# Kernel optimization log

Measured on AMD Instinct MI355X. Metric: run time of the kernel, lower is better.

The kernel has to match this reference:

```python
import jax, jax.numpy as jnp
import numpy as np
from jax import lax

# SRCNN: conv 9x9 (1->64) + ReLU, conv 5x5 (64->32) + ReLU, conv 5x5 (32->1), same padding.
# 13 units total: indices 0-3 (x2 stage), 4-7 (x4 stage), 8-11 (x8 stage), 12 (msf).

def _conv(x, w, b):
    y = lax.conv_general_dilated(x, w, window_strides=(1, 1), padding='SAME',
                                 dimension_numbers=('NCHW', 'OIHW', 'NCHW'))
    return y + b[None, :, None, None]


def _srcnn(x, w1, b1, w2, b2, w3, b3):
    h = jax.nn.relu(_conv(x, w1, b1))
    h = jax.nn.relu(_conv(h, w2, b2))
    return _conv(h, w3, b3)


def _interleave(p0, p1, p2, p3):
    # out[b,c,2h,2w]=p0, out[b,c,2h,2w+1]=p1, out[b,c,2h+1,2w]=p2, out[b,c,2h+1,2w+1]=p3
    B, C, H, W = p0.shape
    x = jnp.stack([jnp.stack([p0, p1], axis=-1),
                   jnp.stack([p2, p3], axis=-1)], axis=-2)  # (B,C,H,W,2,2) dims (b,c,h,w,r,s)
    x = x.transpose(0, 1, 2, 4, 3, 5)                        # (b,c,h,r,w,s)
    return x.reshape(B, C, 2 * H, 2 * W)


def _stage(x, off, W1, B1, W2, B2, W3, B3):
    outs = [_srcnn(x, W1[off + i], B1[off + i], W2[off + i], B2[off + i],
                   W3[off + i], B3[off + i]) for i in range(4)]
    return _interleave(*outs)


def _upscale(x, s):
    B, C, H, W = x.shape
    return jax.image.resize(x, (B, C, H * s, W * s), method='bilinear')


def setup_inputs() -> dict:
    key = jax.random.key(0)
    ks = jax.random.split(key, 7)
    image = jax.random.normal(ks[0], (4, 1, 64, 64), dtype=jnp.float32)
    n = 13
    W1 = jax.random.normal(ks[1], (n, 64, 1, 9, 9), dtype=jnp.float32) * 0.05
    B1 = jnp.zeros((n, 64), dtype=jnp.float32)
    W2 = jax.random.normal(ks[2], (n, 32, 64, 5, 5), dtype=jnp.float32) * 0.05
    B2 = jnp.zeros((n, 32), dtype=jnp.float32)
    W3 = jax.random.normal(ks[3], (n, 1, 32, 5, 5), dtype=jnp.float32) * 0.05
    B3 = jnp.zeros((n, 1), dtype=jnp.float32)
    return {'image': image, 'W1': W1, 'B1': B1, 'W2': W2, 'B2': B2, 'W3': W3, 'B3': B3}


def reference(image, W1, B1, W2, B2, W3, B3):
    out_x2 = _stage(image, 0, W1, B1, W2, B2, W3, B3)   # (B,1,128,128)
    out_x4 = _stage(out_x2, 4, W1, B1, W2, B2, W3, B3)  # (B,1,256,256)
    out_x8 = _stage(out_x4, 8, W1, B1, W2, B2, W3, B3)  # (B,1,512,512)
    msf_in = _upscale(out_x2, 4) + _upscale(out_x4, 2) + out_x8
    msf_out = _srcnn(msf_in, W1[12], B1[12], W2[12], B2[12], W3[12], B3[12])
    return (out_x2, out_x4, out_x8, msf_out)
```

## Files before the change

### kernel.cpp

```cpp
#include <hip/hip_runtime.h>


typedef unsigned short ushort_t;
typedef __attribute__((ext_vector_type(8))) short short8;
typedef __attribute__((ext_vector_type(4))) float f32x4;
typedef __attribute__((ext_vector_type(2))) unsigned int u32x2;

__device__ __forceinline__ float us2f(ushort_t u) { return __uint_as_float(((unsigned int)u) << 16); }
__device__ __forceinline__ ushort_t f2us(float f) {
    unsigned int x = __float_as_uint(f);
    return (ushort_t)((x + 0x7fffu + ((x >> 16) & 1u)) >> 16);
}
__device__ __forceinline__ unsigned int pk_bf16(float lo, float hi) {
    unsigned int r;
    asm("v_cvt_pk_bf16_f32 %0, %1, %2" : "=v"(r) : "v"(lo), "v"(hi));
    return r;
}

#define MFMA16(a, b, c) __builtin_amdgcn_mfma_f32_16x16x32_bf16((a), (b), (c), 0, 0, 0)

__global__ __launch_bounds__(256) void prep_weights(
    const float* __restrict__ W1, const float* __restrict__ W2, const float* __restrict__ W3,
    ushort_t* __restrict__ w1t, ushort_t* __restrict__ w2t, ushort_t* __restrict__ w3t)
{
    int i = blockIdx.x * 256 + threadIdx.x;
    if (i < 13 * 3 * 4 * 64 * 8) {
        int e = i & 7, ch = (i >> 3) & 63, cig = (i >> 9) & 3;
        int r = i >> 11;
        int kc = r % 3, u = r / 3;
        int tap = kc * 32 + e * 4 + cig;
        w1t[i] = (tap < 81) ? f2us(W1[(u * 64 + ch) * 81 + tap]) : (ushort_t)0;
    }
    if (i < 532480) {
        int e = i & 7, co = (i >> 3) & 31, qq = (i >> 8) & 3;
        int b = i >> 10;
        int dy = b % 5, tt = b / 5;
        int c8 = tt % 8, u = tt / 8;
        int ci = c8 * 8 + e;
        int tap = dy * 5 + qq;
        w2t[i] = f2us(W2[((u * 32 + co) * 64 + ci) * 25 + tap]);
    }
    if (i < 133120) {
        int e = i & 7, co = (i >> 3) & 31, cig = (i >> 8) & 3;
        int b = i >> 10;
        int dy = b % 5, s = b / 5;
        int c = s % 2, u = s / 2;
        int ci = c * 32 + cig * 8 + e;
        int tap = dy * 5 + 4;
        w2t[532480 + i] = f2us(W2[((u * 32 + co) * 64 + ci) * 25 + tap]);
    }
    if (i < 13 * 25 * 32) {
        int ci = i & 31, r = i >> 5;
        int tap = r % 25, u = r / 25;
        w3t[i] = f2us(W3[(u * 32 + ci) * 25 + tap]);
    }
}

__global__ __launch_bounds__(256, 2) void srcnn_mfma(
    const float* __restrict__ in, int H, int W,
    const ushort_t* __restrict__ w1t, const ushort_t* __restrict__ w2t,
    const ushort_t* __restrict__ w3t,
    const float* __restrict__ gB1, const float* __restrict__ gB2,
    const float* __restrict__ gB3,
    int unitBase, float* __restrict__ out, int s2)
{
    __shared__ __align__(16) char smem[52928];
    ushort_t* sH1  = (ushort_t*)smem;
    ushort_t* sInU = (ushort_t*)(smem + 51328);
    ushort_t* sW3  = (ushort_t*)(smem + 51328);
    ushort_t* sH2  = (ushort_t*)smem;

    const int t = threadIdx.x, lane = t & 63, wv = t >> 6;
    const int q = lane >> 4, l15 = lane & 15;
    const int z = blockIdx.z;
    const int k4 = (s2 == 2) ? (z >> 2) : 0;
    const int b  = (s2 == 2) ? (z & 3)  : z;
    const int unit = unitBase + k4;
    const int ppx = k4 & 1, ppy = k4 >> 1;
    const int ox0 = blockIdx.x * 12, oy0 = blockIdx.y * 12;
    const int outW = W * s2;
    const int outH = H * s2;
    const float* inb = in + (size_t)b * H * W;

    const char* w2m_u = (const char*)w2t + (size_t)unit * 81920;
    const char* w2x_u = (const char*)w2t + 1064960 + (size_t)unit * 20480;

    auto loadW = [&](short8* buf, const char* base, int blk) {
        const char* g = base + (size_t)blk * 10240 + q * 512 + l15 * 16;
#pragma unroll
        for (int dy = 0; dy < 5; ++dy) {
            buf[dy]     = *(const short8*)(g + dy * 2048);
            buf[5 + dy] = *(const short8*)(g + dy * 2048 + 256);
        }
    };

    for (int idx = t; idx < 784; idx += 256) {
        int y = idx / 28, x = idx - 28 * y;
        int gy = oy0 - 8 + y, gx = ox0 - 8 + x;
        sInU[idx] = (gy >= 0 && gy < H && gx >= 0 && gx < W)
                    ? f2us(inb[(size_t)gy * W + gx]) : (ushort_t)0;
    }
    __syncthreads();

    const ushort_t* w1u = w1t + (size_t)unit * (3 * 4 * 64 * 8);

    f32x4 bias4[4];
#pragma unroll
    for (int n = 0; n < 4; ++n)
        bias4[n] = *(const f32x4*)&gB1[unit * 64 + n * 16 + q * 4];

#pragma unroll 1
    for (int ms = 0; ms < 2; ++ms) {
        const int mbase = ms * 16;
        const int nim = ms ? 3 : 4;
        f32x4 acc1h[4][4];
#pragma unroll
        for (int i = 0; i < 4; ++i)
#pragma unroll
            for (int n = 0; n < 4; ++n) acc1h[i][n] = (f32x4){0.f, 0.f, 0.f, 0.f};

#pragma unroll 1
        for (int kc = 0; kc < 3; ++kc) {
            short8 bh[4];
#pragma unroll
            for (int n = 0; n < 4; ++n)
                bh[n] = *(const short8*)&w1u[((kc * 4 + q) * 64 + n * 16 + l15) * 8];
            int toff8[8];
#pragma unroll
            for (int j = 0; j < 8; ++j) {
                int T = kc * 32 + j * 4 + q;
                int ty = (T * 57) >> 9;
                int o  = ty * 28 + (T - 9 * ty);
                toff8[j] = (T < 81) ? o : 0;
            }
#pragma unroll
            for (int im = 0; im < 4; ++im) {
                if (im < nim) {
                    int m = mbase + wv + im * 4;
                    if (m < 25) {
                        int px = m * 16 + l15;
                        int py1 = (px * 205) >> 12;
                        int base = py1 * 28 + (px - 20 * py1);
                        union { short8 v; ushort_t u[8]; } a;
#pragma unroll
                        for (int j = 0; j < 8; ++j)
                            a.u[j] = sInU[base + toff8[j]];
#pragma unroll
                        for (int n = 0; n < 4; ++n)
                            acc1h[im][n] = MFMA16(bh[n], a.v, acc1h[im][n]);
                    }
                }
            }
        }

#pragma unroll
        for (int im = 0; im < 4; ++im) {
            if (im < nim) {
                int m = mbase + wv + im * 4;
                if (m < 25) {
                    int px = m * 16 + l15;
                    int py1 = (px * 205) >> 12;
                    int px1 = px - 20 * py1;
                    int gy = oy0 - 4 + py1, gx = ox0 - 4 + px1;
                    bool ok = (gy >= 0 && gy < H && gx >= 0 && gx < W);
#pragma unroll
                    for (int n = 0; n < 4; ++n) {
                        float v0 = fmaxf(acc1h[im][n][0] + bias4[n][0], 0.f);
                        float v1 = fmaxf(acc1h[im][n][1] + bias4[n][1], 0.f);
                        float v2 = fmaxf(acc1h[im][n][2] + bias4[n][2], 0.f);
                        float v3 = fmaxf(acc1h[im][n][3] + bias4[n][3], 0.f);
                        unsigned int w0 = pk_bf16(v0, v1);
                        unsigned int w1 = pk_bf16(v2, v3);
                        if (!ok) { w0 = 0u; w1 = 0u; }
                        *(u32x2*)&sH1[(n * 2 + (q >> 1)) * 3208 + px * 8 + (q & 1) * 4]
                            = (u32x2){w0, w1};
                    }
                }
            }
        }
    }
    __syncthreads();

    {
        const ushort_t* w3u = w3t + unit * 800;
        for (int i = t; i < 800; i += 256) sW3[i] = w3u[i];
    }

    f32x4 acc2[4][2];
#pragma unroll
    for (int i = 0; i < 4; ++i) { acc2[i][0] = (f32x4){0.f,0.f,0.f,0.f}; acc2[i][1] = (f32x4){0.f,0.f,0.f,0.f}; }

    {
        short8 Wa[10], Wb[10];
        loadW(Wa, w2m_u, 0);
#pragma unroll
        for (int c8 = 0; c8 < 8; ++c8) {
            const short8* cw = (c8 & 1) ? Wb : Wa;
            short8*       nw = (c8 & 1) ? Wa : Wb;
            if (c8 < 7) loadW(nw, w2m_u, c8 + 1);
            else        loadW(nw, w2x_u, 0);
            const ushort_t* bpl = &sH1[c8 * 3208];
#pragma unroll
            for (int rel = 0; rel < 8; ++rel) {
                int row = wv * 4 + rel;
                short8 bf = *(const short8*)&bpl[(row * 20 + l15 + q) * 8];
                const int dylo = rel - 3 < 0 ? 0 : rel - 3;
                const int dyhi = rel < 4 ? rel : 4;
#pragma unroll
                for (int dy = 0; dy < 5; ++dy) {
                    if (dy >= dylo && dy <= dyhi) {
                        int im = rel - dy;
                        acc2[im][0] = MFMA16(cw[dy],     bf, acc2[im][0]);
                        acc2[im][1] = MFMA16(cw[5 + dy], bf, acc2[im][1]);
                    }
                }
            }
        }
#pragma unroll
        for (int c = 0; c < 2; ++c) {
            const short8* cw = (c & 1) ? Wb : Wa;
            short8*       nw = (c & 1) ? Wa : Wb;
            if (c == 0) loadW(nw, w2x_u, 1);
            const ushort_t* base = &sH1[(c * 4 + q) * 3208];
#pragma unroll
            for (int rel = 0; rel < 8; ++rel) {
                int row = wv * 4 + rel;
                short8 bf = *(const short8*)&base[(row * 20 + l15 + 4) * 8];
                const int dylo = rel - 3 < 0 ? 0 : rel - 3;
                const int dyhi = rel < 4 ? rel : 4;
#pragma unroll
                for (int dy = 0; dy < 5; ++dy) {
                    if (dy >= dylo && dy <= dyhi) {
                        int im = rel - dy;
                        acc2[im][0] = MFMA16(cw[dy],     bf, acc2[im][0]);
                        acc2[im][1] = MFMA16(cw[5 + dy], bf, acc2[im][1]);
                    }
                }
            }
        }
    }
    __syncthreads();

    {
        f32x4 b2v[2];
#pragma unroll
        for (int n = 0; n < 2; ++n)
            b2v[n] = *(const f32x4*)&gB2[unit * 32 + n * 16 + q * 4];
        int gx = ox0 - 2 + l15;
        bool okx = (gx >= 0 && gx < W);
#pragma unroll
        for (int im = 0; im < 4; ++im) {
            int hy = wv * 4 + im;
            int gy = oy0 - 2 + hy;
            bool ok = okx && (gy >= 0 && gy < H);
#pragma unroll
            for (int n = 0; n < 2; ++n) {
                float v0 = fmaxf(acc2[im][n][0] + b2v[n][0], 0.f);
                float v1 = fmaxf(acc2[im][n][1] + b2v[n][1], 0.f);
                float v2 = fmaxf(acc2[im][n][2] + b2v[n][2], 0.f);
                float v3 = fmaxf(acc2[im][n][3] + b2v[n][3], 0.f);
                unsigned int w0 = pk_bf16(v0, v1);
                unsigned int w1 = pk_bf16(v2, v3);
                if (!ok) { w0 = 0u; w1 = 0u; }
                *(u32x2*)&sH2[(n * 2 + (q >> 1)) * 2064 + (hy * 16 + l15) * 8 + (q & 1) * 4]
                    = (u32x2){w0, w1};
            }
        }
    }
    __syncthreads();

    float b3 = gB3[unit];
    const int nm = (wv == 0) ? 3 : 2;
    int oyj[3], oxj[3];
#pragma unroll
    for (int jm = 0; jm < 3; ++jm) {
        int p = (wv + 4 * jm) * 16 + l15;
        oyj[jm] = (p * 683) >> 13;
        oxj[jm] = p - 12 * oyj[jm];
    }
    f32x4 acc3[3];
#pragma unroll
    for (int jm = 0; jm < 3; ++jm) acc3[jm] = (f32x4){0.f, 0.f, 0.f, 0.f};

#pragma unroll 1
    for (int tap = 0; tap < 25; ++tap) {
        int dy = (tap * 13) >> 6, dx = tap - 5 * dy;
        short8 w = *(const short8*)&sW3[tap * 32 + q * 8];
#pragma unroll
        for (int jm = 0; jm < 3; ++jm) {
            if (jm < nm) {
                int h2px = (oyj[jm] + dy) * 16 + oxj[jm] + dx;
                short8 a = *(const short8*)&sH2[q * 2064 + h2px * 8];
                acc3[jm] = MFMA16(a, w, acc3[jm]);
            }
        }
    }
    if (l15 == 0) {
#pragma unroll
        for (int jm = 0; jm < 3; ++jm) {
            if (jm < nm) {
                int mt = wv + 4 * jm;
#pragma unroll
                for (int r = 0; r < 4; ++r) {
                    int pp = mt * 16 + q * 4 + r;
                    int oy = (pp * 683) >> 13, ox = pp - 12 * oy;
                    int gy = oy0 + oy, gx = ox0 + ox;
                    if (gy < H && gx < W) {
                        size_t o = (size_t)b * outW * outH + (size_t)(gy * s2 + ppy) * outW + (gx * s2 + ppx);
                        out[o] = acc3[jm][r] + b3;
                    }
                }
            }
        }
    }
}

__device__ __forceinline__ void ax_w(int i, float inv_s, int n, int& i0, int& i1, float& w1) {
    float c  = (i + 0.5f) * inv_s - 0.5f;
    float fl = floorf(c);
    w1 = c - fl;
    int ii = (int)fl;
    i0 = ii < 0 ? 0 : ii;
    i1 = (ii + 1 >= n) ? (n - 1) : (ii + 1);
}

__global__ __launch_bounds__(256) void msf_in_kernel(
    const float* __restrict__ f2, const float* __restrict__ f4,
    const float* __restrict__ f8, float* __restrict__ dst)
{
    int idx = blockIdx.x * 256 + threadIdx.x;
    int x = idx & 511;
    int y = (idx >> 9) & 511;
    int b = idx >> 18;

    int y0, y1, x0, x1;
    float wy, wx;

    ax_w(y, 0.25f, 128, y0, y1, wy);
    ax_w(x, 0.25f, 128, x0, x1, wx);
    const float* p2 = f2 + (size_t)b * 16384;
    float v4 = (1.f - wy) * ((1.f - wx) * p2[y0 * 128 + x0] + wx * p2[y0 * 128 + x1])
             +        wy  * ((1.f - wx) * p2[y1 * 128 + x0] + wx * p2[y1 * 128 + x1]);

    ax_w(y, 0.5f, 256, y0, y1, wy);
    ax_w(x, 0.5f, 256, x0, x1, wx);
    const float* p4 = f4 + (size_t)b * 65536;
    float v2 = (1.f - wy) * ((1.f - wx) * p4[y0 * 256 + x0] + wx * p4[y0 * 256 + x1])
             +        wy  * ((1.f - wx) * p4[y1 * 256 + x0] + wx * p4[y1 * 256 + x1]);

    dst[idx] = v4 + v2 + f8[idx];
}

extern "C" void kernel_launch(void* const* d_in, const int* in_sizes, int n_in,
                              void* d_out, int out_size, void* d_ws, size_t ws_size,
                              hipStream_t stream)
{
    (void)in_sizes; (void)n_in; (void)out_size; (void)ws_size;

    const float* image = (const float*)d_in[0];
    const float* W1    = (const float*)d_in[1];
    const float* B1    = (const float*)d_in[2];
    const float* W2    = (const float*)d_in[3];
    const float* B2    = (const float*)d_in[4];
    const float* W3    = (const float*)d_in[5];
    const float* B3    = (const float*)d_in[6];

    float* out = (float*)d_out;
    float* o2 = out;
    float* o4 = out + 65536;
    float* o8 = out + 327680;
    float* om = out + 1376256;

    float*    fm  = (float*)d_ws;
    ushort_t* w1t = (ushort_t*)((char*)d_ws + 4194304);
    ushort_t* w2t = (ushort_t*)((char*)d_ws + 4354048);
    ushort_t* w3t = (ushort_t*)((char*)d_ws + 5685248);

    prep_weights<<<2600, 256, 0, stream>>>(W1, W2, W3, w1t, w2t, w3t);

    srcnn_mfma<<<dim3(6, 6, 16), 256, 0, stream>>>(
        image, 64, 64, w1t, w2t, w3t, B1, B2, B3, 0, o2, 2);
    srcnn_mfma<<<dim3(11, 11, 16), 256, 0, stream>>>(
        o2, 128, 128, w1t, w2t, w3t, B1, B2, B3, 4, o4, 2);
    srcnn_mfma<<<dim3(22, 22, 16), 256, 0, stream>>>(
        o4, 256, 256, w1t, w2t, w3t, B1, B2, B3, 8, o8, 2);
    msf_in_kernel<<<4096, 256, 0, stream>>>(o2, o4, o8, fm);
    srcnn_mfma<<<dim3(43, 43, 4), 256, 0, stream>>>(
        fm, 512, 512, w1t, w2t, w3t, B1, B2, B3, 12, om, 1);
}
```

Before: 626.1 us.

## Double block to 512 threads and split conv2 output channels across wave halves

```diff
diff --git a/kernel.cpp b/kernel.cpp
--- a/kernel.cpp
+++ b/kernel.cpp
@@ -56,7 +56,7 @@
     }
 }
 
-__global__ __launch_bounds__(256, 2) void srcnn_mfma(
+__global__ __launch_bounds__(512, 2) void srcnn_mfma(
     const float* __restrict__ in, int H, int W,
     const ushort_t* __restrict__ w1t, const ushort_t* __restrict__ w2t,
     const ushort_t* __restrict__ w3t,
@@ -72,6 +72,7 @@
 
     const int t = threadIdx.x, lane = t & 63, wv = t >> 6;
     const int q = lane >> 4, l15 = lane & 15;
+    const int wp = wv & 3, nh = wv >> 2;
     const int z = blockIdx.z;
     const int k4 = (s2 == 2) ? (z >> 2) : 0;
     const int b  = (s2 == 2) ? (z & 3)  : z;
@@ -85,16 +86,14 @@
     const char* w2m_u = (const char*)w2t + (size_t)unit * 81920;
     const char* w2x_u = (const char*)w2t + 1064960 + (size_t)unit * 20480;
 
-    auto loadW = [&](short8* buf, const char* base, int blk) {
-        const char* g = base + (size_t)blk * 10240 + q * 512 + l15 * 16;
-#pragma unroll
-        for (int dy = 0; dy < 5; ++dy) {
-            buf[dy]     = *(const short8*)(g + dy * 2048);
-            buf[5 + dy] = *(const short8*)(g + dy * 2048 + 256);
-        }
+    auto loadW5 = [&](short8* buf, const char* base, int blk) {
+        const char* g = base + (size_t)blk * 10240 + q * 512 + nh * 256 + l15 * 16;
+#pragma unroll
+        for (int dy = 0; dy < 5; ++dy)
+            buf[dy] = *(const short8*)(g + dy * 2048);
     };
 
-    for (int idx = t; idx < 784; idx += 256) {
+    for (int idx = t; idx < 784; idx += 512) {
         int y = idx / 28, x = idx - 28 * y;
         int gy = oy0 - 8 + y, gx = ox0 - 8 + x;
         sInU[idx] = (gy >= 0 && gy < H && gx >= 0 && gx < W)
@@ -109,10 +108,8 @@
     for (int n = 0; n < 4; ++n)
         bias4[n] = *(const f32x4*)&gB1[unit * 64 + n * 16 + q * 4];
 
-#pragma unroll 1
-    for (int ms = 0; ms < 2; ++ms) {
-        const int mbase = ms * 16;
-        const int nim = ms ? 3 : 4;
+    const int nim1 = (wv == 0) ? 4 : 3;
+    {
         f32x4 acc1h[4][4];
 #pragma unroll
         for (int i = 0; i < 4; ++i)
@@ -135,46 +132,42 @@
             }
 #pragma unroll
             for (int im = 0; im < 4; ++im) {
-                if (im < nim) {
-                    int m = mbase + wv + im * 4;
-                    if (m < 25) {
-                        int px = m * 16 + l15;
-                        int py1 = (px * 205) >> 12;
-                        int base = py1 * 28 + (px - 20 * py1);
-                        union { short8 v; ushort_t u[8]; } a;
-#pragma unroll
-                        for (int j = 0; j < 8; ++j)
-                            a.u[j] = sInU[base + toff8[j]];
-#pragma unroll
-                        for (int n = 0; n < 4; ++n)
-                            acc1h[im][n] = MFMA16(bh[n], a.v, acc1h[im][n]);
-                    }
-                }
-            }
-        }
-
-#pragma unroll
-        for (int im = 0; im < 4; ++im) {
-            if (im < nim) {
-                int m = mbase + wv + im * 4;
-                if (m < 25) {
+                if (im < nim1) {
+                    int m = wv + im * 8;
                     int px = m * 16 + l15;
                     int py1 = (px * 205) >> 12;
-                    int px1 = px - 20 * py1;
-                    int gy = oy0 - 4 + py1, gx = ox0 - 4 + px1;
-                    bool ok = (gy >= 0 && gy < H && gx >= 0 && gx < W);
-#pragma unroll
-                    for (int n = 0; n < 4; ++n) {
-                        float v0 = fmaxf(acc1h[im][n][0] + bias4[n][0], 0.f);
-                        float v1 = fmaxf(acc1h[im][n][1] + bias4[n][1], 0.f);
-                        float v2 = fmaxf(acc1h[im][n][2] + bias4[n][2], 0.f);
-                        float v3 = fmaxf(acc1h[im][n][3] + bias4[n][3], 0.f);
-                        unsigned int w0 = pk_bf16(v0, v1);
-                        unsigned int w1 = pk_bf16(v2, v3);
-                        if (!ok) { w0 = 0u; w1 = 0u; }
-                        *(u32x2*)&sH1[(n * 2 + (q >> 1)) * 3208 + px * 8 + (q & 1) * 4]
-                            = (u32x2){w0, w1};
-                    }
+                    int base = py1 * 28 + (px - 20 * py1);
+                    union { short8 v; ushort_t u[8]; } a;
+#pragma unroll
+                    for (int j = 0; j < 8; ++j)
+                        a.u[j] = sInU[base + toff8[j]];
+#pragma unroll
+                    for (int n = 0; n < 4; ++n)
+                        acc1h[im][n] = MFMA16(bh[n], a.v, acc1h[im][n]);
+                }
+            }
+        }
+
+#pragma unroll
+        for (int im = 0; im < 4; ++im) {
+            if (im < nim1) {
+                int m = wv + im * 8;
+                int px = m * 16 + l15;
+                int py1 = (px * 205) >> 12;
+                int px1 = px - 20 * py1;
+                int gy = oy0 - 4 + py1, gx = ox0 - 4 + px1;
+                bool ok = (gy >= 0 && gy < H && gx >= 0 && gx < W);
+#pragma unroll
+                for (int n = 0; n < 4; ++n) {
+                    float v0 = fmaxf(acc1h[im][n][0] + bias4[n][0], 0.f);
+                    float v1 = fmaxf(acc1h[im][n][1] + bias4[n][1], 0.f);
+                    float v2 = fmaxf(acc1h[im][n][2] + bias4[n][2], 0.f);
+                    float v3 = fmaxf(acc1h[im][n][3] + bias4[n][3], 0.f);
+                    unsigned int w0 = pk_bf16(v0, v1);
+                    unsigned int w1 = pk_bf16(v2, v3);
+                    if (!ok) { w0 = 0u; w1 = 0u; }
+                    *(u32x2*)&sH1[(n * 2 + (q >> 1)) * 3208 + px * 8 + (q & 1) * 4]
+                        = (u32x2){w0, w1};
                 }
             }
         }
@@ -183,26 +176,26 @@
 
     {
         const ushort_t* w3u = w3t + unit * 800;
-        for (int i = t; i < 800; i += 256) sW3[i] = w3u[i];
-    }
-
-    f32x4 acc2[4][2];
-#pragma unroll
-    for (int i = 0; i < 4; ++i) { acc2[i][0] = (f32x4){0.f,0.f,0.f,0.f}; acc2[i][1] = (f32x4){0.f,0.f,0.f,0.f}; }
+        for (int i = t; i < 800; i += 512) sW3[i] = w3u[i];
+    }
+
+    f32x4 acc2[4];
+#pragma unroll
+    for (int i = 0; i < 4; ++i) acc2[i] = (f32x4){0.f, 0.f, 0.f, 0.f};
 
     {
-        short8 Wa[10], Wb[10];
-        loadW(Wa, w2m_u, 0);
+        short8 Wa[5], Wb[5];
+        loadW5(Wa, w2m_u, 0);
 #pragma unroll
         for (int c8 = 0; c8 < 8; ++c8) {
             const short8* cw = (c8 & 1) ? Wb : Wa;
             short8*       nw = (c8 & 1) ? Wa : Wb;
-            if (c8 < 7) loadW(nw, w2m_u, c8 + 1);
-            else        loadW(nw, w2x_u, 0);
+            if (c8 < 7) loadW5(nw, w2m_u, c8 + 1);
+            else        loadW5(nw, w2x_u, 0);
             const ushort_t* bpl = &sH1[c8 * 3208];
 #pragma unroll
             for (int rel = 0; rel < 8; ++rel) {
-                int row = wv * 4 + rel;
+                int row = wp * 4 + rel;
                 short8 bf = *(const short8*)&bpl[(row * 20 + l15 + q) * 8];
                 const int dylo = rel - 3 < 0 ? 0 : rel - 3;
                 const int dyhi = rel < 4 ? rel : 4;
@@ -210,8 +203,7 @@
                 for (int dy = 0; dy < 5; ++dy) {
                     if (dy >= dylo && dy <= dyhi) {
                         int im = rel - dy;
-                        acc2[im][0] = MFMA16(cw[dy],     bf, acc2[im][0]);
-                        acc2[im][1] = MFMA16(cw[5 + dy], bf, acc2[im][1]);
+                        acc2[im] = MFMA16(cw[dy], bf, acc2[im]);
                     }
                 }
             }
@@ -220,11 +212,11 @@
         for (int c = 0; c < 2; ++c) {
             const short8* cw = (c & 1) ? Wb : Wa;
             short8*       nw = (c & 1) ? Wa : Wb;
-            if (c == 0) loadW(nw, w2x_u, 1);
+            if (c == 0) loadW5(nw, w2x_u, 1);
             const ushort_t* base = &sH1[(c * 4 + q) * 3208];
 #pragma unroll
             for (int rel = 0; rel < 8; ++rel) {
-                int row = wv * 4 + rel;
+                int row = wp * 4 + rel;
                 short8 bf = *(const short8*)&base[(row * 20 + l15 + 4) * 8];
                 const int dylo = rel - 3 < 0 ? 0 : rel - 3;
                 const int dyhi = rel < 4 ? rel : 4;
@@ -232,8 +224,7 @@
                 for (int dy = 0; dy < 5; ++dy) {
                     if (dy >= dylo && dy <= dyhi) {
                         int im = rel - dy;
-                        acc2[im][0] = MFMA16(cw[dy],     bf, acc2[im][0]);
-                        acc2[im][1] = MFMA16(cw[5 + dy], bf, acc2[im][1]);
+                        acc2[im] = MFMA16(cw[dy], bf, acc2[im]);
                     }
                 }
             }
@@ -242,52 +233,46 @@
     __syncthreads();
 
     {
-        f32x4 b2v[2];
-#pragma unroll
-        for (int n = 0; n < 2; ++n)
-            b2v[n] = *(const f32x4*)&gB2[unit * 32 + n * 16 + q * 4];
+        f32x4 b2v = *(const f32x4*)&gB2[unit * 32 + nh * 16 + q * 4];
         int gx = ox0 - 2 + l15;
         bool okx = (gx >= 0 && gx < W);
 #pragma unroll
         for (int im = 0; im < 4; ++im) {
-            int hy = wv * 4 + im;
+            int hy = wp * 4 + im;
             int gy = oy0 - 2 + hy;
             bool ok = okx && (gy >= 0 && gy < H);
-#pragma unroll
-            for (int n = 0; n < 2; ++n) {
-                float v0 = fmaxf(acc2[im][n][0] + b2v[n][0], 0.f);
-                float v1 = fmaxf(acc2[im][n][1] + b2v[n][1], 0.f);
-                float v2 = fmaxf(acc2[im][n][2] + b2v[n][2], 0.f);
-                float v3 = fmaxf(acc2[im][n][3] + b2v[n][3], 0.f);
-                unsigned int w0 = pk_bf16(v0, v1);
-                unsigned int w1 = pk_bf16(v2, v3);
-                if (!ok) { w0 = 0u; w1 = 0u; }
-                *(u32x2*)&sH2[(n * 2 + (q >> 1)) * 2064 + (hy * 16 + l15) * 8 + (q & 1) * 4]
-                    = (u32x2){w0, w1};
-            }
+            float v0 = fmaxf(acc2[im][0] + b2v[0], 0.f);
+            float v1 = fmaxf(acc2[im][1] + b2v[1], 0.f);
+            float v2 = fmaxf(acc2[im][2] + b2v[2], 0.f);
+            float v3 = fmaxf(acc2[im][3] + b2v[3], 0.f);
+            unsigned int w0 = pk_bf16(v0, v1);
+            unsigned int w1 = pk_bf16(v2, v3);
+            if (!ok) { w0 = 0u; w1 = 0u; }
+            *(u32x2*)&sH2[(nh * 2 + (q >> 1)) * 2064 + (hy * 16 + l15) * 8 + (q & 1) * 4]
+                = (u32x2){w0, w1};
         }
     }
     __syncthreads();
 
     float b3 = gB3[unit];
-    const int nm = (wv == 0) ? 3 : 2;
-    int oyj[3], oxj[3];
-#pragma unroll
-    for (int jm = 0; jm < 3; ++jm) {
-        int p = (wv + 4 * jm) * 16 + l15;
+    const int nm = (wv == 0) ? 2 : 1;
+    int oyj[2], oxj[2];
+#pragma unroll
+    for (int jm = 0; jm < 2; ++jm) {
+        int p = (wv + 8 * jm) * 16 + l15;
         oyj[jm] = (p * 683) >> 13;
         oxj[jm] = p - 12 * oyj[jm];
     }
-    f32x4 acc3[3];
-#pragma unroll
-    for (int jm = 0; jm < 3; ++jm) acc3[jm] = (f32x4){0.f, 0.f, 0.f, 0.f};
+    f32x4 acc3[2];
+#pragma unroll
+    for (int jm = 0; jm < 2; ++jm) acc3[jm] = (f32x4){0.f, 0.f, 0.f, 0.f};
 
 #pragma unroll 1
     for (int tap = 0; tap < 25; ++tap) {
         int dy = (tap * 13) >> 6, dx = tap - 5 * dy;
         short8 w = *(const short8*)&sW3[tap * 32 + q * 8];
 #pragma unroll
-        for (int jm = 0; jm < 3; ++jm) {
+        for (int jm = 0; jm < 2; ++jm) {
             if (jm < nm) {
                 int h2px = (oyj[jm] + dy) * 16 + oxj[jm] + dx;
                 short8 a = *(const short8*)&sH2[q * 2064 + h2px * 8];
@@ -297,9 +282,9 @@
     }
     if (l15 == 0) {
 #pragma unroll
-        for (int jm = 0; jm < 3; ++jm) {
+        for (int jm = 0; jm < 2; ++jm) {
             if (jm < nm) {
-                int mt = wv + 4 * jm;
+                int mt = wv + 8 * jm;
 #pragma unroll
                 for (int r = 0; r < 4; ++r) {
                     int pp = mt * 16 + q * 4 + r;
@@ -378,13 +363,13 @@
 
     prep_weights<<<2600, 256, 0, stream>>>(W1, W2, W3, w1t, w2t, w3t);
 
-    srcnn_mfma<<<dim3(6, 6, 16), 256, 0, stream>>>(
+    srcnn_mfma<<<dim3(6, 6, 16), 512, 0, stream>>>(
         image, 64, 64, w1t, w2t, w3t, B1, B2, B3, 0, o2, 2);
-    srcnn_mfma<<<dim3(11, 11, 16), 256, 0, stream>>>(
+    srcnn_mfma<<<dim3(11, 11, 16), 512, 0, stream>>>(
         o2, 128, 128, w1t, w2t, w3t, B1, B2, B3, 4, o4, 2);
-    srcnn_mfma<<<dim3(22, 22, 16), 256, 0, stream>>>(
+    srcnn_mfma<<<dim3(22, 22, 16), 512, 0, stream>>>(
         o4, 256, 256, w1t, w2t, w3t, B1, B2, B3, 8, o8, 2);
     msf_in_kernel<<<4096, 256, 0, stream>>>(o2, o4, o8, fm);
-    srcnn_mfma<<<dim3(43, 43, 4), 256, 0, stream>>>(
+    srcnn_mfma<<<dim3(43, 43, 4), 512, 0, stream>>>(
         fm, 512, 512, w1t, w2t, w3t, B1, B2, B3, 12, om, 1);
 }
```

New measurement: 824.5 us. 31.7% more time.

## Split conv1 channels into two halves to halve shared memory footprint

Applied to the files above, without the earlier changes.

```diff
diff --git a/kernel.cpp b/kernel.cpp
--- a/kernel.cpp
+++ b/kernel.cpp
@@ -64,10 +64,10 @@
     const float* __restrict__ gB3,
     int unitBase, float* __restrict__ out, int s2)
 {
-    __shared__ __align__(16) char smem[52928];
-    ushort_t* sH1  = (ushort_t*)smem;
-    ushort_t* sInU = (ushort_t*)(smem + 51328);
-    ushort_t* sW3  = (ushort_t*)(smem + 51328);
+    __shared__ __align__(16) char smem[27264];
+    ushort_t* sH1h = (ushort_t*)smem;
+    ushort_t* sInU = (ushort_t*)(smem + 25664);
+    ushort_t* sW3  = (ushort_t*)(smem + 25664);
     ushort_t* sH2  = (ushort_t*)smem;
 
     const int t = threadIdx.x, lane = t & 63, wv = t >> 6;
@@ -104,142 +104,145 @@
 
     const ushort_t* w1u = w1t + (size_t)unit * (3 * 4 * 64 * 8);
 
-    f32x4 bias4[4];
-#pragma unroll
-    for (int n = 0; n < 4; ++n)
-        bias4[n] = *(const f32x4*)&gB1[unit * 64 + n * 16 + q * 4];
+    f32x4 acc2[4][2];
+#pragma unroll
+    for (int i = 0; i < 4; ++i) { acc2[i][0] = (f32x4){0.f,0.f,0.f,0.f}; acc2[i][1] = (f32x4){0.f,0.f,0.f,0.f}; }
 
 #pragma unroll 1
-    for (int ms = 0; ms < 2; ++ms) {
-        const int mbase = ms * 16;
-        const int nim = ms ? 3 : 4;
-        f32x4 acc1h[4][4];
-#pragma unroll
-        for (int i = 0; i < 4; ++i)
-#pragma unroll
-            for (int n = 0; n < 4; ++n) acc1h[i][n] = (f32x4){0.f, 0.f, 0.f, 0.f};
+    for (int h = 0; h < 2; ++h) {
+        {
+            f32x4 bias4[2];
+#pragma unroll
+            for (int n = 0; n < 2; ++n)
+                bias4[n] = *(const f32x4*)&gB1[unit * 64 + (h * 2 + n) * 16 + q * 4];
 
 #pragma unroll 1
-        for (int kc = 0; kc < 3; ++kc) {
-            short8 bh[4];
-#pragma unroll
-            for (int n = 0; n < 4; ++n)
-                bh[n] = *(const short8*)&w1u[((kc * 4 + q) * 64 + n * 16 + l15) * 8];
-            int toff8[8];
-#pragma unroll
-            for (int j = 0; j < 8; ++j) {
-                int T = kc * 32 + j * 4 + q;
-                int ty = (T * 57) >> 9;
-                int o  = ty * 28 + (T - 9 * ty);
-                toff8[j] = (T < 81) ? o : 0;
-            }
-#pragma unroll
-            for (int im = 0; im < 4; ++im) {
-                if (im < nim) {
-                    int m = mbase + wv + im * 4;
-                    if (m < 25) {
-                        int px = m * 16 + l15;
-                        int py1 = (px * 205) >> 12;
-                        int base = py1 * 28 + (px - 20 * py1);
-                        union { short8 v; ushort_t u[8]; } a;
-#pragma unroll
-                        for (int j = 0; j < 8; ++j)
-                            a.u[j] = sInU[base + toff8[j]];
-#pragma unroll
-                        for (int n = 0; n < 4; ++n)
-                            acc1h[im][n] = MFMA16(bh[n], a.v, acc1h[im][n]);
-                    }
-                }
-            }
-        }
-
-#pragma unroll
-        for (int im = 0; im < 4; ++im) {
-            if (im < nim) {
-                int m = mbase + wv + im * 4;
-                if (m < 25) {
-                    int px = m * 16 + l15;
-                    int py1 = (px * 205) >> 12;
-                    int px1 = px - 20 * py1;
-                    int gy = oy0 - 4 + py1, gx = ox0 - 4 + px1;
-                    bool ok = (gy >= 0 && gy < H && gx >= 0 && gx < W);
-#pragma unroll
-                    for (int n = 0; n < 4; ++n) {
-                        float v0 = fmaxf(acc1h[im][n][0] + bias4[n][0], 0.f);
-                        float v1 = fmaxf(acc1h[im][n][1] + bias4[n][1], 0.f);
-                        float v2 = fmaxf(acc1h[im][n][2] + bias4[n][2], 0.f);
-                        float v3 = fmaxf(acc1h[im][n][3] + bias4[n][3], 0.f);
-                        unsigned int w0 = pk_bf16(v0, v1);
-                        unsigned int w1 = pk_bf16(v2, v3);
-                        if (!ok) { w0 = 0u; w1 = 0u; }
-                        *(u32x2*)&sH1[(n * 2 + (q >> 1)) * 3208 + px * 8 + (q & 1) * 4]
-                            = (u32x2){w0, w1};
-                    }
-                }
-            }
-        }
-    }
-    __syncthreads();
-
-    {
-        const ushort_t* w3u = w3t + unit * 800;
-        for (int i = t; i < 800; i += 256) sW3[i] = w3u[i];
-    }
-
-    f32x4 acc2[4][2];
-#pragma unroll
-    for (int i = 0; i < 4; ++i) { acc2[i][0] = (f32x4){0.f,0.f,0.f,0.f}; acc2[i][1] = (f32x4){0.f,0.f,0.f,0.f}; }
-
-    {
-        short8 Wa[10], Wb[10];
-        loadW(Wa, w2m_u, 0);
-#pragma unroll
-        for (int c8 = 0; c8 < 8; ++c8) {
-            const short8* cw = (c8 & 1) ? Wb : Wa;
-            short8*       nw = (c8 & 1) ? Wa : Wb;
-            if (c8 < 7) loadW(nw, w2m_u, c8 + 1);
-            else        loadW(nw, w2x_u, 0);
-            const ushort_t* bpl = &sH1[c8 * 3208];
-#pragma unroll
-            for (int rel = 0; rel < 8; ++rel) {
-                int row = wv * 4 + rel;
-                short8 bf = *(const short8*)&bpl[(row * 20 + l15 + q) * 8];
-                const int dylo = rel - 3 < 0 ? 0 : rel - 3;
-                const int dyhi = rel < 4 ? rel : 4;
-#pragma unroll
-                for (int dy = 0; dy < 5; ++dy) {
-                    if (dy >= dylo && dy <= dyhi) {
-                        int im = rel - dy;
-                        acc2[im][0] = MFMA16(cw[dy],     bf, acc2[im][0]);
-                        acc2[im][1] = MFMA16(cw[5 + dy], bf, acc2[im][1]);
-                    }
-                }
-            }
-        }
-#pragma unroll
-        for (int c = 0; c < 2; ++c) {
-            const short8* cw = (c & 1) ? Wb : Wa;
-            short8*       nw = (c & 1) ? Wa : Wb;
-            if (c == 0) loadW(nw, w2x_u, 1);
-            const ushort_t* base = &sH1[(c * 4 + q) * 3208];
-#pragma unroll
-            for (int rel = 0; rel < 8; ++rel) {
-                int row = wv * 4 + rel;
-                short8 bf = *(const short8*)&base[(row * 20 + l15 + 4) * 8];
-                const int dylo = rel - 3 < 0 ? 0 : rel - 3;
-                const int dyhi = rel < 4 ? rel : 4;
-#pragma unroll
-                for (int dy = 0; dy < 5; ++dy) {
-                    if (dy >= dylo && dy <= dyhi) {
-                        int im = rel - dy;
-                        acc2[im][0] = MFMA16(cw[dy],     bf, acc2[im][0]);
-                        acc2[im][1] = MFMA16(cw[5 + dy], bf, acc2[im][1]);
-                    }
-                }
-            }
-        }
-    }
-    __syncthreads();
+            for (int ms = 0; ms < 2; ++ms) {
+                const int mbase = ms * 16;
+                const int nim = ms ? 3 : 4;
+                f32x4 acc1h[4][2];
+#pragma unroll
+                for (int i = 0; i < 4; ++i) {
+                    acc1h[i][0] = (f32x4){0.f,0.f,0.f,0.f};
+                    acc1h[i][1] = (f32x4){0.f,0.f,0.f,0.f};
+                }
+
+#pragma unroll 1
+                for (int kc = 0; kc < 3; ++kc) {
+                    short8 bh[2];
+#pragma unroll
+                    for (int n = 0; n < 2; ++n)
+                        bh[n] = *(const short8*)&w1u[((kc * 4 + q) * 64 + (h * 2 + n) * 16 + l15) * 8];
+                    int toff8[8];
+#pragma unroll
+                    for (int j = 0; j < 8; ++j) {
+                        int T = kc * 32 + j * 4 + q;
+                        int ty = (T * 57) >> 9;
+                        int o  = ty * 28 + (T - 9 * ty);
+                        toff8[j] = (T < 81) ? o : 0;
+                    }
+#pragma unroll
+                    for (int im = 0; im < 4; ++im) {
+                        if (im < nim) {
+                            int m = mbase + wv + im * 4;
+                            if (m < 25) {
+                                int px = m * 16 + l15;
+                                int py1 = (px * 205) >> 12;
+                                int base = py1 * 28 + (px - 20 * py1);
+                                union { short8 v; ushort_t u[8]; } a;
+#pragma unroll
+                                for (int j = 0; j < 8; ++j)
+                                    a.u[j] = sInU[base + toff8[j]];
+#pragma unroll
+                                for (int n = 0; n < 2; ++n)
+                                    acc1h[im][n] = MFMA16(bh[n], a.v, acc1h[im][n]);
+                            }
+                        }
+                    }
+                }
+
+#pragma unroll
+                for (int im = 0; im < 4; ++im) {
+                    if (im < nim) {
+                        int m = mbase + wv + im * 4;
+                        if (m < 25) {
+                            int px = m * 16 + l15;
+                            int py1 = (px * 205) >> 12;
+                            int px1 = px - 20 * py1;
+                            int gy = oy0 - 4 + py1, gx = ox0 - 4 + px1;
+                            bool ok = (gy >= 0 && gy < H && gx >= 0 && gx < W);
+#pragma unroll
+                            for (int n = 0; n < 2; ++n) {
+                                float v0 = fmaxf(acc1h[im][n][0] + bias4[n][0], 0.f);
+                                float v1 = fmaxf(acc1h[im][n][1] + bias4[n][1], 0.f);
+                                float v2 = fmaxf(acc1h[im][n][2] + bias4[n][2], 0.f);
+                                float v3 = fmaxf(acc1h[im][n][3] + bias4[n][3], 0.f);
+                                unsigned int w0 = pk_bf16(v0, v1);
+                                unsigned int w1 = pk_bf16(v2, v3);
+                                if (!ok) { w0 = 0u; w1 = 0u; }
+                                *(u32x2*)&sH1h[(n * 2 + (q >> 1)) * 3208 + px * 8 + (q & 1) * 4]
+                                    = (u32x2){w0, w1};
+                            }
+                        }
+                    }
+                }
+            }
+        }
+        __syncthreads();
+
+        if (h == 1) {
+            const ushort_t* w3u = w3t + unit * 800;
+            for (int i = t; i < 800; i += 256) sW3[i] = w3u[i];
+        }
+
+        {
+            short8 Wa[10], Wb[10];
+            loadW(Wa, w2m_u, h * 4);
+#pragma unroll
+            for (int c8l = 0; c8l < 4; ++c8l) {
+                const short8* cw = (c8l & 1) ? Wb : Wa;
+                short8*       nw = (c8l & 1) ? Wa : Wb;
+                if (c8l < 3) loadW(nw, w2m_u, h * 4 + c8l + 1);
+                else         loadW(nw, w2x_u, h);
+                const ushort_t* bpl = &sH1h[c8l * 3208];
+#pragma unroll
+                for (int rel = 0; rel < 8; ++rel) {
+                    int row = wv * 4 + rel;
+                    short8 bf = *(const short8*)&bpl[(row * 20 + l15 + q) * 8];
+                    const int dylo = rel - 3 < 0 ? 0 : rel - 3;
+                    const int dyhi = rel < 4 ? rel : 4;
+#pragma unroll
+                    for (int dy = 0; dy < 5; ++dy) {
+                        if (dy >= dylo && dy <= dyhi) {
+                            int im = rel - dy;
+                            acc2[im][0] = MFMA16(cw[dy],     bf, acc2[im][0]);
+                            acc2[im][1] = MFMA16(cw[5 + dy], bf, acc2[im][1]);
+                        }
+                    }
+                }
+            }
+            {
+                const short8* cw = Wa;
+                const ushort_t* base = &sH1h[q * 3208];
+#pragma unroll
+                for (int rel = 0; rel < 8; ++rel) {
+                    int row = wv * 4 + rel;
+                    short8 bf = *(const short8*)&base[(row * 20 + l15 + 4) * 8];
+                    const int dylo = rel - 3 < 0 ? 0 : rel - 3;
+                    const int dyhi = rel < 4 ? rel : 4;
+#pragma unroll
+                    for (int dy = 0; dy < 5; ++dy) {
+                        if (dy >= dylo && dy <= dyhi) {
+                            int im = rel - dy;
+                            acc2[im][0] = MFMA16(cw[dy],     bf, acc2[im][0]);
+                            acc2[im][1] = MFMA16(cw[5 + dy], bf, acc2[im][1]);
+                        }
+                    }
+                }
+            }
+        }
+        __syncthreads();
+    }
 
     {
         f32x4 b2v[2];
```

New measurement: 687.2 us. 9.8% more time.
